# Kernel tuning notes

Measured on AMD Instinct MI355X. Metric: run time of the kernel, lower is better.

Reference implementation:

```python
import jax, jax.numpy as jnp
import numpy as np

N_EMBD = 2048
HIDDEN = 2 * N_EMBD        # 4096
ADAPT = HIDDEN // 16       # 256
B, S = 4, 2048


def _layernorm(x, g, b, eps=1e-5):
    mu = jnp.mean(x, axis=-1, keepdims=True)
    var = jnp.var(x, axis=-1, keepdims=True)
    return (x - mu) * jax.lax.rsqrt(var + eps) * g + b


def setup_inputs() -> dict:
    key = jax.random.key(0)
    ks = jax.random.split(key, 7)
    scale = 1.0 / np.sqrt(N_EMBD)
    adapt_scale = scale * 0.01
    return {
        "x": jax.random.normal(ks[0], (B, S, N_EMBD), dtype=jnp.float32),
        "W_up": jax.random.normal(ks[1], (HIDDEN, N_EMBD), dtype=jnp.float32) * scale,
        "W_gate": jax.random.normal(ks[2], (HIDDEN, N_EMBD), dtype=jnp.float32) * scale,
        "W_down": jax.random.normal(ks[3], (N_EMBD, HIDDEN), dtype=jnp.float32) * scale,
        "W_pre": jax.random.normal(ks[4], (ADAPT, N_EMBD), dtype=jnp.float32) * adapt_scale,
        "W_post": jax.random.normal(ks[5], (ADAPT, HIDDEN), dtype=jnp.float32) * adapt_scale,
        "W_proj": jax.random.normal(ks[6], (HIDDEN, ADAPT), dtype=jnp.float32) * adapt_scale,
        "ln_g": jnp.ones((ADAPT,), dtype=jnp.float32),
        "ln_b": jnp.zeros((ADAPT,), dtype=jnp.float32),
    }


def reference(x, W_up, W_gate, W_down, W_pre, W_post, W_proj, ln_g, ln_b):
    # SwiGLU trunk
    up = jnp.einsum('bsd,hd->bsh', x, W_up)
    gate = jnp.einsum('bsd,hd->bsh', x, W_gate)
    hidden = jax.nn.silu(gate) * up                      # [B,S,H]
    # Low-rank quadratic adapter
    adapt_in = _layernorm(jnp.einsum('bsd,ad->bsa', x, W_pre), ln_g, ln_b)       # [B,S,A]
    adapt_out = _layernorm(jnp.einsum('bsh,ah->bsa', hidden, W_post), ln_g, ln_b)  # [B,S,A]
    aw = jnp.einsum('bsa,bta->bst', adapt_in, adapt_out)  # [B,S,S]
    aw = jax.nn.silu(jnp.clip(aw, -5.0, 5.0))
    adapt = jnp.einsum('bst,bta->bsa', aw, adapt_in)      # [B,S,A]
    adapt = 0.1 * jnp.einsum('bsa,ha->bsh', adapt, W_proj)
    hidden = hidden + adapt
    out = jnp.einsum('bsh,dh->bsd', hidden, W_down)       # dropout p=0 -> identity
    return out
```

## Files before the change

### kernel.cpp

```cpp
#include <hip/hip_runtime.h>
#include <cstdint>
#include <cstddef>

typedef unsigned short u16;
typedef short short8 __attribute__((ext_vector_type(8)));
typedef float f32x4 __attribute__((ext_vector_type(4)));

__device__ __forceinline__ u16 f2bf(float f) {
  union { float f; unsigned u; } x; x.f = f;
  unsigned r = x.u + 0x7FFFu + ((x.u >> 16) & 1u);
  return (u16)(r >> 16);
}
__device__ __forceinline__ float b2f(u16 h) {
  union { unsigned u; float f; } x; x.u = ((unsigned)h) << 16;
  return x.f;
}
__device__ __forceinline__ float silu_f(float v) {
  return v / (1.f + __expf(-v));
}
__device__ __forceinline__ void gll(const u16* g, u16* l) {
  __builtin_amdgcn_global_load_lds((const __attribute__((address_space(1))) unsigned*)g,
                                   (__attribute__((address_space(3))) unsigned*)l, 16, 0, 0);
}

__global__ __launch_bounds__(256) void cvt7_k(const float4* __restrict__ s0,
                                              const float4* __restrict__ s1,
                                              const float4* __restrict__ s2,
                                              const float4* __restrict__ s3,
                                              const float4* __restrict__ s4,
                                              const float4* __restrict__ s5,
                                              const float4* __restrict__ s6,
                                              ushort4* __restrict__ dst) {
  const int i = blockIdx.x * 256 + threadIdx.x;
  const int o1 = 4194304, o2 = 6291456, o3 = 8388608, o4 = 10485760,
            o5 = 10616832, o6 = 10878976, o7 = 11141120;
  if (i >= o7) return;
  const float4* src;
  int base;
  if      (i < o1) { src = s0; base = 0;  }
  else if (i < o2) { src = s1; base = o1; }
  else if (i < o3) { src = s2; base = o2; }
  else if (i < o4) { src = s3; base = o3; }
  else if (i < o5) { src = s4; base = o4; }
  else if (i < o6) { src = s5; base = o5; }
  else             { src = s6; base = o6; }
  float4 v = src[i - base];
  ushort4 o;
  o.x = f2bf(v.x); o.y = f2bf(v.y); o.z = f2bf(v.z); o.w = f2bf(v.w);
  dst[i] = o;
}

__global__ __launch_bounds__(256) void red_ln_k(const float* __restrict__ part,
                                                const float* __restrict__ g,
                                                const float* __restrict__ b,
                                                u16* __restrict__ out,
                                                u16* __restrict__ outT, int Mtot) {
  const int row = blockIdx.x;
  const int a = threadIdx.x;
  const size_t stride = (size_t)Mtot * 256;
  const size_t base = (size_t)row * 256 + a;
  float v = part[base] + part[base + stride] + part[base + 2 * stride] + part[base + 3 * stride];
  float s = v, s2 = v * v;
#pragma unroll
  for (int o = 32; o; o >>= 1) { s += __shfl_down(s, o, 64); s2 += __shfl_down(s2, o, 64); }
  __shared__ float red[8];
  int l = a & 63, w = a >> 6;
  if (l == 0) { red[w] = s; red[4 + w] = s2; }
  __syncthreads();
  s  = red[0] + red[1] + red[2] + red[3];
  s2 = red[4] + red[5] + red[6] + red[7];
  float mu  = s * 0.00390625f;
  float var = s2 * 0.00390625f - mu * mu;
  float rs  = rsqrtf(var + 1e-5f);
  float o   = (v - mu) * rs * g[a] + b[a];
  u16 ob = f2bf(o);
  out[base] = ob;
  if (outT) {
    int bi = row >> 11, t = row & 2047;
    outT[((size_t)bi * 256 + a) * 2048 + t] = ob;
  }
}

__global__ __launch_bounds__(256) void red_k(const float* __restrict__ part,
                                             u16* __restrict__ out, int Mtot) {
  const int row = blockIdx.x;
  const int a = threadIdx.x;
  const size_t stride = (size_t)Mtot * 256;
  const size_t base = (size_t)row * 256 + a;
  float v = part[base] + part[base + stride] + part[base + 2 * stride] + part[base + 3 * stride];
  out[base] = f2bf(v);
}

template <int EPI>
__global__ __launch_bounds__(256) void gemm_bt(const u16* __restrict__ A,
                                               const u16* __restrict__ B,
                                               void* __restrict__ Cv,
                                               int M, int N, int K,
                                               long bA, long bB, long bC) {
  __shared__ u16 Al[128 * 64];
  __shared__ u16 Bl[128 * 64];
  const int tid  = threadIdx.x;
  const int bz   = blockIdx.z;
  const int brow = blockIdx.y * 128;
  const int bcol = blockIdx.x * 128;
  A += (size_t)bz * bA;
  B += (size_t)bz * bB;
  const int lane = tid & 63;
  const int w = tid >> 6, wr = w >> 1, wc = w & 1;
  const int srow = tid >> 3;
  const int scol = (tid & 7) * 8;

  f32x4 acc[4][4] = {};

  for (int kt = 0; kt < K; kt += 64) {
#pragma unroll
    for (int i = 0; i < 4; ++i)
      gll(A + (size_t)(brow + i * 32 + srow) * K + kt + scol, &Al[(i * 256 + tid) * 8]);
#pragma unroll
    for (int i = 0; i < 4; ++i)
      gll(B + (size_t)(bcol + i * 32 + srow) * K + kt + scol, &Bl[(i * 256 + tid) * 8]);
    __syncthreads();
#pragma unroll
    for (int kk = 0; kk < 2; ++kk) {
      short8 af[4], bfr[4];
      const int ko = kk * 32 + (lane >> 4) * 8;
#pragma unroll
      for (int m = 0; m < 4; ++m)
        af[m] = *(const short8*)&Al[(wr * 64 + m * 16 + (lane & 15)) * 64 + ko];
#pragma unroll
      for (int n = 0; n < 4; ++n)
        bfr[n] = *(const short8*)&Bl[(wc * 64 + n * 16 + (lane & 15)) * 64 + ko];
#pragma unroll
      for (int m = 0; m < 4; ++m)
#pragma unroll
        for (int n = 0; n < 4; ++n)
          acc[m][n] = __builtin_amdgcn_mfma_f32_16x16x32_bf16(af[m], bfr[n], acc[m][n], 0, 0, 0);
    }
    __syncthreads();
  }

  const int col0 = bcol + wc * 64 + (lane & 15);
  const int row0 = brow + wr * 64 + ((lane >> 4) << 2);
  u16* Cb = (u16*)Cv + (size_t)bz * bC;
#pragma unroll
  for (int m = 0; m < 4; ++m)
#pragma unroll
    for (int j = 0; j < 4; ++j) {
      size_t roff = (size_t)(row0 + m * 16 + j) * N + col0;
#pragma unroll
      for (int n = 0; n < 4; ++n) {
        float v = acc[m][n][j];
        if (EPI == 2) {
          v = fminf(5.f, fmaxf(-5.f, v));
          v = silu_f(v);
        }
        Cb[roff + n * 16] = f2bf(v);
      }
    }
}

__global__ __launch_bounds__(256) void gemm_sk(const u16* __restrict__ A,
                                               const u16* __restrict__ B,
                                               float* __restrict__ part,
                                               int M, int N, int Kfull, int Kc,
                                               long bA, long bB, int Mtot) {
  const int z  = blockIdx.z;
  const int b  = z >> 2, sk = z & 3;
  const int brow = blockIdx.y * 128;
  const int bcol = blockIdx.x * 128;
  A += (size_t)b * bA + (size_t)sk * Kc;
  B += (size_t)b * bB + (size_t)sk * Kc;

  __shared__ u16 Al[128 * 64];
  __shared__ u16 Bl[128 * 64];
  const int tid  = threadIdx.x;
  const int lane = tid & 63;
  const int w = tid >> 6, wr = w >> 1, wc = w & 1;
  const int srow = tid >> 3;
  const int scol = (tid & 7) * 8;

  f32x4 acc[4][4] = {};

  for (int kt = 0; kt < Kc; kt += 64) {
#pragma unroll
    for (int i = 0; i < 4; ++i)
      gll(A + (size_t)(brow + i * 32 + srow) * Kfull + kt + scol, &Al[(i * 256 + tid) * 8]);
#pragma unroll
    for (int i = 0; i < 4; ++i)
      gll(B + (size_t)(bcol + i * 32 + srow) * Kfull + kt + scol, &Bl[(i * 256 + tid) * 8]);
    __syncthreads();
#pragma unroll
    for (int kk = 0; kk < 2; ++kk) {
      short8 af[4], bfr[4];
      const int ko = kk * 32 + (lane >> 4) * 8;
#pragma unroll
      for (int m = 0; m < 4; ++m)
        af[m] = *(const short8*)&Al[(wr * 64 + m * 16 + (lane & 15)) * 64 + ko];
#pragma unroll
      for (int n = 0; n < 4; ++n)
        bfr[n] = *(const short8*)&Bl[(wc * 64 + n * 16 + (lane & 15)) * 64 + ko];
#pragma unroll
      for (int m = 0; m < 4; ++m)
#pragma unroll
        for (int n = 0; n < 4; ++n)
          acc[m][n] = __builtin_amdgcn_mfma_f32_16x16x32_bf16(af[m], bfr[n], acc[m][n], 0, 0, 0);
    }
    __syncthreads();
  }

  const int col0 = bcol + wc * 64 + (lane & 15);
  const int row0 = brow + wr * 64 + ((lane >> 4) << 2);
  float* P = part + ((size_t)sk * Mtot + (size_t)b * M) * N;
#pragma unroll
  for (int m = 0; m < 4; ++m)
#pragma unroll
    for (int j = 0; j < 4; ++j) {
      size_t roff = (size_t)(row0 + m * 16 + j) * N + col0;
#pragma unroll
      for (int n = 0; n < 4; ++n) P[roff + n * 16] = acc[m][n][j];
    }
}

template <int EPI>
__global__ __launch_bounds__(512, 2) void gemm256(const u16* __restrict__ A,
                                                  const u16* __restrict__ B,
                                                  void* __restrict__ Cv,
                                                  const u16* __restrict__ H,
                                                  int M, int N, int K,
                                                  long bA, long bB, long bC) {
  __shared__ __align__(16) u16 As[32768];
  __shared__ __align__(16) u16 Bs[32768];

  const int tid = threadIdx.x;
  const int bz  = blockIdx.z;
  A += (size_t)bz * bA;
  B += (size_t)bz * bB;

  const int gx = gridDim.x;
  const int nwg = gx * gridDim.y;
  int orig = blockIdx.y * gx + blockIdx.x;
  {
    int q = nwg >> 3, r = nwg & 7;
    int xcd = orig & 7, idx = orig >> 3;
    orig = (xcd < r) ? xcd * (q + 1) + idx : r * (q + 1) + (xcd - r) * q + idx;
  }
  const int brow = (orig / gx) * 256;
  const int bcol = (orig % gx) * 256;

  const int lane = tid & 63;
  const int wid  = tid >> 6;
  const int wm = wid >> 2, wn = wid & 3;

  const int srow   = tid >> 2;
  const int schunk = (((tid & 3) ^ ((tid >> 3) & 3)) << 3);
  const u16* Asrc = A + (size_t)(brow + srow) * K + schunk;
  const u16* Bsrc = B + (size_t)(bcol + srow) * K + schunk;
  const int sdst = tid * 8;

  const int fr  = lane & 15;
  const int rc8 = (((lane >> 4) ^ ((lane >> 1) & 3)) << 3);
  const int aoff0 = (wm * 128 + fr) * 32 + rc8;
  const int boff0 = (wn * 64 + fr) * 32 + rc8;

  const int NT = K >> 6;
  f32x4 acc[8][4] = {};

  auto stA = [&](int tt, int kq) {
    u16* d = &As[(((tt & 1) * 2 + kq) << 13) + sdst];
    const u16* s = Asrc + (size_t)(tt << 6) + kq * 32;
    gll(s, d); gll(s + (size_t)128 * K, d + 4096);
  };
  auto stB = [&](int tt, int kq) {
    u16* d = &Bs[(((tt & 1) * 2 + kq) << 13) + sdst];
    const u16* s = Bsrc + (size_t)(tt << 6) + kq * 32;
    gll(s, d); gll(s + (size_t)128 * K, d + 4096);
  };

  stA(0, 0); stB(0, 0); stA(0, 1); stB(0, 1); stA(1, 0); stB(1, 0);
  asm volatile("s_waitcnt vmcnt(8)" ::: "memory");
  __builtin_amdgcn_s_barrier();

#define PH_READ_A(kqbase, mlo)                                                   \
  {                                                                              \
    _Pragma("unroll")                                                            \
    for (int m = 0; m < 4; ++m)                                                  \
      af[m] = *(const short8*)(kqbase + aoff0 + (mlo + m) * 512);                \
  }
#define PH_READ_B(kqbase)                                                        \
  {                                                                              \
    _Pragma("unroll")                                                            \
    for (int n = 0; n < 4; ++n)                                                  \
      bf[n] = *(const short8*)(kqbase + boff0 + n * 512);                        \
  }
#define PH_MFMA(mlo)                                                             \
  __builtin_amdgcn_s_barrier();                                                  \
  asm volatile("s_waitcnt lgkmcnt(0)" ::: "memory");                             \
  __builtin_amdgcn_s_setprio(1);                                                 \
  {                                                                              \
    _Pragma("unroll")                                                            \
    for (int m = 0; m < 4; ++m)                                                  \
      _Pragma("unroll")                                                          \
      for (int n = 0; n < 4; ++n)                                                \
        acc[mlo + m][n] =                                                        \
            __builtin_amdgcn_mfma_f32_16x16x32_bf16(af[m], bf[n], acc[mlo + m][n], 0, 0, 0); \
  }                                                                              \
  __builtin_amdgcn_s_setprio(0);

  int t = 0;
  for (; t < NT - 3; ++t) {
    const int cur = t & 1;
    const u16* a0 = &As[(cur * 2) << 13];
    const u16* b0 = &Bs[(cur * 2) << 13];
    const u16* a1 = a0 + 8192;
    const u16* b1 = b0 + 8192;
    short8 af[4], bf[4];

    PH_READ_A(a0, 0) PH_READ_B(b0)
    stA(t + 1, 1);
    PH_MFMA(0)
    __builtin_amdgcn_s_barrier();

    PH_READ_A(a0, 4)
    stB(t + 1, 1);
    PH_MFMA(4)
    asm volatile("s_waitcnt vmcnt(8)" ::: "memory");
    __builtin_amdgcn_s_barrier();

    PH_READ_A(a1, 0) PH_READ_B(b1)
    stA(t + 2, 0);
    PH_MFMA(0)
    __builtin_amdgcn_s_barrier();

    PH_READ_A(a1, 4)
    stB(t + 2, 0);
    PH_MFMA(4)
    asm volatile("s_waitcnt vmcnt(8)" ::: "memory");
    __builtin_amdgcn_s_barrier();
  }
  for (; t < NT; ++t) {
    const int cur = t & 1;
    const u16* a0 = &As[(cur * 2) << 13];
    const u16* b0 = &Bs[(cur * 2) << 13];
    const u16* a1 = a0 + 8192;
    const u16* b1 = b0 + 8192;
    short8 af[4], bf[4];

    PH_READ_A(a0, 0) PH_READ_B(b0)
    if (t + 1 < NT) stA(t + 1, 1);
    PH_MFMA(0)
    __builtin_amdgcn_s_barrier();

    PH_READ_A(a0, 4)
    if (t + 1 < NT) stB(t + 1, 1);
    PH_MFMA(4)
    asm volatile("s_waitcnt vmcnt(0)" ::: "memory");
    __builtin_amdgcn_s_barrier();

    PH_READ_A(a1, 0) PH_READ_B(b1)
    if (t + 2 < NT) stA(t + 2, 0);
    PH_MFMA(0)
    __builtin_amdgcn_s_barrier();

    PH_READ_A(a1, 4)
    if (t + 2 < NT) stB(t + 2, 0);
    PH_MFMA(4)
    asm volatile("s_waitcnt vmcnt(0)" ::: "memory");
    __builtin_amdgcn_s_barrier();
  }
#undef PH_READ_A
#undef PH_READ_B
#undef PH_MFMA

  const int col0 = bcol + wn * 64 + fr;
  const int row0 = brow + wm * 128 + ((lane >> 4) << 2);

  if (EPI == 0) {
    float* Cf = (float*)Cv + (size_t)bz * bC;
#pragma unroll
    for (int m = 0; m < 8; ++m)
#pragma unroll
      for (int j = 0; j < 4; ++j) {
        size_t roff = (size_t)(row0 + m * 16 + j) * N + col0;
#pragma unroll
        for (int n = 0; n < 4; ++n) Cf[roff + n * 16] = acc[m][n][j];
      }
  } else if (EPI == 1) {
    u16* Cb = (u16*)Cv + (size_t)bz * bC;
#pragma unroll
    for (int m = 0; m < 8; ++m)
#pragma unroll
      for (int j = 0; j < 4; ++j) {
        size_t roff = (size_t)(row0 + m * 16 + j) * N + col0;
#pragma unroll
        for (int n = 0; n < 4; ++n) Cb[roff + n * 16] = f2bf(acc[m][n][j]);
      }
  } else if (EPI == 2) {
    u16* Cb = (u16*)Cv + (size_t)bz * bC;
#pragma unroll
    for (int m = 0; m < 8; ++m)
#pragma unroll
      for (int j = 0; j < 4; ++j) {
        size_t roff = (size_t)(row0 + m * 16 + j) * N + col0;
#pragma unroll
        for (int n = 0; n < 4; ++n) {
          float v = acc[m][n][j];
          v = fminf(5.f, fmaxf(-5.f, v));
          Cb[roff + n * 16] = f2bf(silu_f(v));
        }
      }
  } else if (EPI == 3) {
    u16* Cb = (u16*)Cv + (size_t)bz * bC;
    const u16* Hb = H + (size_t)bz * bC;
#pragma unroll
    for (int m = 0; m < 8; ++m)
#pragma unroll
      for (int j = 0; j < 4; ++j) {
        size_t roff = (size_t)(row0 + m * 16 + j) * N + col0;
#pragma unroll
        for (int n = 0; n < 4; ++n) {
          size_t idx = roff + n * 16;
          Cb[idx] = f2bf(b2f(Hb[idx]) + 0.1f * acc[m][n][j]);
        }
      }
  } else {
    u16* Cb = (u16*)Cv + (size_t)bz * bC;
    const u16* Hb = H + (size_t)bz * bC;
#pragma unroll
    for (int m = 0; m < 8; ++m)
#pragma unroll
      for (int j = 0; j < 4; ++j) {
        size_t roff = (size_t)(row0 + m * 16 + j) * N + col0;
#pragma unroll
        for (int n = 0; n < 4; ++n) {
          size_t idx = roff + n * 16;
          Cb[idx] = f2bf(silu_f(acc[m][n][j]) * b2f(Hb[idx]));
        }
      }
  }
}

extern "C" void kernel_launch(void* const* d_in, const int* in_sizes, int n_in,
                              void* d_out, int out_size, void* d_ws, size_t ws_size,
                              hipStream_t stream) {
  const float* x      = (const float*)d_in[0];
  const float* W_up   = (const float*)d_in[1];
  const float* W_gate = (const float*)d_in[2];
  const float* W_down = (const float*)d_in[3];
  const float* W_pre  = (const float*)d_in[4];
  const float* W_post = (const float*)d_in[5];
  const float* W_proj = (const float*)d_in[6];
  const float* ln_g   = (const float*)d_in[7];
  const float* ln_b   = (const float*)d_in[8];
  (void)in_sizes; (void)n_in; (void)out_size; (void)ws_size;

  const int D = 2048, Hh = 4096, A_ = 256, Bn = 4, S = 2048, M = 8192;

  char* p = (char*)d_ws;
  u16* xb      = (u16*)p; p += (size_t)M * D * 2;
  u16* Wup_b   = (u16*)p; p += (size_t)Hh * D * 2;
  u16* Wgate_b = (u16*)p; p += (size_t)Hh * D * 2;
  u16* Wdown_b = (u16*)p; p += (size_t)D * Hh * 2;
  u16* Wpre_b  = (u16*)p; p += (size_t)A_ * D * 2;
  u16* Wpost_b = (u16*)p; p += (size_t)A_ * Hh * 2;
  u16* Wproj_b = (u16*)p; p += (size_t)Hh * A_ * 2;
  u16* hidden  = (u16*)p; p += (size_t)M * Hh * 2;
  u16* scratch = (u16*)p; p += (size_t)M * Hh * 2;
  char* q = (char*)scratch;
  u16*   aw        = (u16*)q; q += (size_t)Bn * S * S * 2;
  u16*   adapt_in  = (u16*)q; q += (size_t)M * A_ * 2;
  u16*   adapt_inT = (u16*)q; q += (size_t)M * A_ * 2;
  u16*   adapt_out = (u16*)q; q += (size_t)M * A_ * 2;
  u16*   adaptb    = (u16*)q; q += (size_t)M * A_ * 2;
  float* part = (float*)Wup_b;

  cvt7_k<<<dim3(43520), dim3(256), 0, stream>>>((const float4*)x, (const float4*)W_up,
                                                (const float4*)W_gate, (const float4*)W_down,
                                                (const float4*)W_pre, (const float4*)W_post,
                                                (const float4*)W_proj, (ushort4*)xb);

  gemm256<1><<<dim3(Hh / 256, M / 256, 1), 512, 0, stream>>>(xb, Wup_b, hidden, nullptr,
                                                             M, Hh, D, 0, 0, 0);
  gemm256<4><<<dim3(Hh / 256, M / 256, 1), 512, 0, stream>>>(xb, Wgate_b, hidden, hidden,
                                                             M, Hh, D, 0, 0, 0);

  gemm_sk<<<dim3(A_ / 128, M / 128, 4), 256, 0, stream>>>(xb, Wpre_b, part,
                                                          M, A_, D, D / 4, 0, 0, M);
  red_ln_k<<<dim3(M), 256, 0, stream>>>(part, ln_g, ln_b, adapt_in, adapt_inT, M);

  gemm_sk<<<dim3(A_ / 128, M / 128, 4), 256, 0, stream>>>(hidden, Wpost_b, part,
                                                          M, A_, Hh, Hh / 4, 0, 0, M);
  red_ln_k<<<dim3(M), 256, 0, stream>>>(part, ln_g, ln_b, adapt_out, nullptr, M);

  gemm_bt<2><<<dim3(S / 128, S / 128, Bn), 256, 0, stream>>>(adapt_in, adapt_out, aw,
                                                             S, S, A_,
                                                             (long)S * A_, (long)S * A_, (long)S * S);

  gemm_sk<<<dim3(A_ / 128, S / 128, Bn * 4), 256, 0, stream>>>(aw, adapt_inT, part,
                                                               S, A_, S, S / 4,
                                                               (long)S * S, (long)A_ * S, M);
  red_k<<<dim3(M), 256, 0, stream>>>(part, adaptb, M);

  gemm256<3><<<dim3(Hh / 256, M / 256, 1), 512, 0, stream>>>(adaptb, Wproj_b, hidden, hidden,
                                                             M, Hh, A_, 0, 0, 0);

  gemm256<0><<<dim3(D / 256, M / 256, 1), 512, 0, stream>>>(hidden, Wdown_b, d_out, nullptr,
                                                            M, D, Hh, 0, 0, 0);
}
```

Before: 635.6 us.

## Restructure GEMM mainloop with register double-buffering and per-half LDS tiles

Rewrites the 256x256 bf16 GEMM main loop. The LDS tile layout changes from K-split 32-column chunks to row-half 64-column tiles with a new XOR swizzle. Fragments are now double-buffered in registers, so LDS reads for the next MFMA group are issued while the current group runs. The whole next K-tile is prefetched in one stage, with fewer barriers per iteration. The goal is to hide LDS latency and barrier stalls, but the prefetch now runs only one tile ahead with a full vmcnt(0) wait, and register pressure rises.

```diff
diff --git a/kernel.cpp b/kernel.cpp
--- a/kernel.cpp
+++ b/kernel.cpp
@@ -251,125 +251,105 @@
   const int wid  = tid >> 6;
   const int wm = wid >> 2, wn = wid & 3;
 
-  const int srow   = tid >> 2;
-  const int schunk = (((tid & 3) ^ ((tid >> 3) & 3)) << 3);
-  const u16* Asrc = A + (size_t)(brow + srow) * K + schunk;
-  const u16* Bsrc = B + (size_t)(bcol + srow) * K + schunk;
-  const int sdst = tid * 8;
+  const int srow = tid >> 3;
+  const int scol = ((((tid & 7) << 4) ^ ((srow & 7) << 4)) >> 1);
+  const u16* Abase = A + (size_t)(brow + srow) * K + scol;
+  const u16* Bbase = B + (size_t)(bcol + srow) * K + scol;
 
   const int fr  = lane & 15;
-  const int rc8 = (((lane >> 4) ^ ((lane >> 1) & 3)) << 3);
-  const int aoff0 = (wm * 128 + fr) * 32 + rc8;
-  const int boff0 = (wn * 64 + fr) * 32 + rc8;
+  const int cs0 = ((((lane >> 4) << 4) ^ ((lane & 7) << 4)) >> 1);
+  const int cs1 = cs0 ^ 32;
+  const int bro = (wn & 1) * 64;
 
   const int NT = K >> 6;
   f32x4 acc[8][4] = {};
 
-  auto stA = [&](int tt, int kq) {
-    u16* d = &As[(((tt & 1) * 2 + kq) << 13) + sdst];
-    const u16* s = Asrc + (size_t)(tt << 6) + kq * 32;
-    gll(s, d); gll(s + (size_t)128 * K, d + 4096);
+  auto stageAll = [&](int tt) {
+    const int ktn = tt << 6;
+    const int bb = (tt & 1) * 2;
+#pragma unroll
+    for (int h = 0; h < 2; ++h) {
+      const u16* s = Abase + (size_t)(h * 128) * K + ktn;
+      u16* d = &As[(bb + h) * 8192 + tid * 8];
+      gll(s, d); gll(s + (size_t)64 * K, d + 4096);
+    }
+#pragma unroll
+    for (int h = 0; h < 2; ++h) {
+      const u16* s = Bbase + (size_t)(h * 128) * K + ktn;
+      u16* d = &Bs[(bb + h) * 8192 + tid * 8];
+      gll(s, d); gll(s + (size_t)64 * K, d + 4096);
+    }
   };
-  auto stB = [&](int tt, int kq) {
-    u16* d = &Bs[(((tt & 1) * 2 + kq) << 13) + sdst];
-    const u16* s = Bsrc + (size_t)(tt << 6) + kq * 32;
-    gll(s, d); gll(s + (size_t)128 * K, d + 4096);
-  };
-
-  stA(0, 0); stB(0, 0); stA(0, 1); stB(0, 1); stA(1, 0); stB(1, 0);
-  asm volatile("s_waitcnt vmcnt(8)" ::: "memory");
+
+#define RD_A(DST, BASE, ROFF, CS)                                           \
+  {                                                                         \
+    _Pragma("unroll")                                                       \
+    for (int m = 0; m < 4; ++m)                                             \
+      DST[m] = *(const short8*)(BASE + (ROFF + m * 16 + fr) * 64 + CS);     \
+  }
+#define RD_B(DST, BASE, CS)                                                 \
+  {                                                                         \
+    _Pragma("unroll")                                                       \
+    for (int n = 0; n < 4; ++n)                                             \
+      DST[n] = *(const short8*)(BASE + (bro + n * 16 + fr) * 64 + CS);      \
+  }
+#define MFMA16(AB, AR, BR)                                                  \
+  __builtin_amdgcn_sched_barrier(0);                                        \
+  __builtin_amdgcn_s_setprio(1);                                            \
+  {                                                                         \
+    _Pragma("unroll")                                                       \
+    for (int m = 0; m < 4; ++m)                                             \
+      _Pragma("unroll")                                                     \
+      for (int n = 0; n < 4; ++n)                                           \
+        acc[AB + m][n] = __builtin_amdgcn_mfma_f32_16x16x32_bf16(           \
+            AR[m], BR[n], acc[AB + m][n], 0, 0, 0);                         \
+  }                                                                         \
+  __builtin_amdgcn_s_setprio(0);                                            \
+  __builtin_amdgcn_sched_barrier(0);
+
+  short8 aR0[4], aR1[4], bR0[4], bR1[4];
+
+  stageAll(0);
+  asm volatile("s_waitcnt vmcnt(0)" ::: "memory");
   __builtin_amdgcn_s_barrier();
-
-#define PH_READ_A(kqbase, mlo)                                                   \
-  {                                                                              \
-    _Pragma("unroll")                                                            \
-    for (int m = 0; m < 4; ++m)                                                  \
-      af[m] = *(const short8*)(kqbase + aoff0 + (mlo + m) * 512);                \
-  }
-#define PH_READ_B(kqbase)                                                        \
-  {                                                                              \
-    _Pragma("unroll")                                                            \
-    for (int n = 0; n < 4; ++n)                                                  \
-      bf[n] = *(const short8*)(kqbase + boff0 + n * 512);                        \
-  }
-#define PH_MFMA(mlo)                                                             \
-  __builtin_amdgcn_s_barrier();                                                  \
-  asm volatile("s_waitcnt lgkmcnt(0)" ::: "memory");                             \
-  __builtin_amdgcn_s_setprio(1);                                                 \
-  {                                                                              \
-    _Pragma("unroll")                                                            \
-    for (int m = 0; m < 4; ++m)                                                  \
-      _Pragma("unroll")                                                          \
-      for (int n = 0; n < 4; ++n)                                                \
-        acc[mlo + m][n] =                                                        \
-            __builtin_amdgcn_mfma_f32_16x16x32_bf16(af[m], bf[n], acc[mlo + m][n], 0, 0, 0); \
-  }                                                                              \
-  __builtin_amdgcn_s_setprio(0);
-
-  int t = 0;
-  for (; t < NT - 3; ++t) {
+  {
+    const u16* aH = &As[wm * 8192];
+    const u16* bH = &Bs[(wn >> 1) * 8192];
+    RD_A(aR0, aH, 0, cs0)
+    RD_B(bR0, bH, cs0)
+  }
+
+  for (int t = 0; t < NT; ++t) {
     const int cur = t & 1;
-    const u16* a0 = &As[(cur * 2) << 13];
-    const u16* b0 = &Bs[(cur * 2) << 13];
-    const u16* a1 = a0 + 8192;
-    const u16* b1 = b0 + 8192;
-    short8 af[4], bf[4];
-
-    PH_READ_A(a0, 0) PH_READ_B(b0)
-    stA(t + 1, 1);
-    PH_MFMA(0)
-    __builtin_amdgcn_s_barrier();
-
-    PH_READ_A(a0, 4)
-    stB(t + 1, 1);
-    PH_MFMA(4)
-    asm volatile("s_waitcnt vmcnt(8)" ::: "memory");
-    __builtin_amdgcn_s_barrier();
-
-    PH_READ_A(a1, 0) PH_READ_B(b1)
-    stA(t + 2, 0);
-    PH_MFMA(0)
-    __builtin_amdgcn_s_barrier();
-
-    PH_READ_A(a1, 4)
-    stB(t + 2, 0);
-    PH_MFMA(4)
-    asm volatile("s_waitcnt vmcnt(8)" ::: "memory");
-    __builtin_amdgcn_s_barrier();
-  }
-  for (; t < NT; ++t) {
-    const int cur = t & 1;
-    const u16* a0 = &As[(cur * 2) << 13];
-    const u16* b0 = &Bs[(cur * 2) << 13];
-    const u16* a1 = a0 + 8192;
-    const u16* b1 = b0 + 8192;
-    short8 af[4], bf[4];
-
-    PH_READ_A(a0, 0) PH_READ_B(b0)
-    if (t + 1 < NT) stA(t + 1, 1);
-    PH_MFMA(0)
-    __builtin_amdgcn_s_barrier();
-
-    PH_READ_A(a0, 4)
-    if (t + 1 < NT) stB(t + 1, 1);
-    PH_MFMA(4)
+    const u16* aH  = &As[(cur * 2 + wm) * 8192];
+    const u16* bH  = &Bs[(cur * 2 + (wn >> 1)) * 8192];
+    const u16* aHn = &As[((cur ^ 1) * 2 + wm) * 8192];
+    const u16* bHn = &Bs[((cur ^ 1) * 2 + (wn >> 1)) * 8192];
+    const bool pf = (t + 1 < NT);
+
+    if (pf) stageAll(t + 1);
+    RD_A(aR1, aH, 64, cs0)
+    MFMA16(0, aR0, bR0)
+
+    RD_A(aR0, aH, 0, cs1)
+    RD_B(bR1, bH, cs1)
+    MFMA16(4, aR1, bR0)
+
+    RD_A(aR1, aH, 64, cs1)
+    MFMA16(0, aR0, bR1)
     asm volatile("s_waitcnt vmcnt(0)" ::: "memory");
     __builtin_amdgcn_s_barrier();
 
-    PH_READ_A(a1, 0) PH_READ_B(b1)
-    if (t + 2 < NT) stA(t + 2, 0);
-    PH_MFMA(0)
+    if (pf) {
+      RD_A(aR0, aHn, 0, cs0)
+      RD_B(bR0, bHn, cs0)
+    }
+    MFMA16(4, aR1, bR1)
     __builtin_amdgcn_s_barrier();
-
-    PH_READ_A(a1, 4)
-    if (t + 2 < NT) stB(t + 2, 0);
-    PH_MFMA(4)
-    asm volatile("s_waitcnt vmcnt(0)" ::: "memory");
-    __builtin_amdgcn_s_barrier();
-  }
-#undef PH_READ_A
-#undef PH_READ_B
-#undef PH_MFMA
+  }
+#undef RD_A
+#undef RD_B
+#undef MFMA16
 
   const int col0 = bcol + wn * 64 + fr;
   const int row0 = brow + wm * 128 + ((lane >> 4) << 2);
```

New measurement: 632.6 us. Within noise of the previous version (-0.5%).
